# Optimization experiments

Hardware: AMD Instinct MI355X
Metric: run time of the kernel (lower is better)

## Reference

```python
import jax, jax.numpy as jnp
import numpy as np

B, S, D, E, F = 2, 2048, 1024, 8, 4096


def setup_inputs() -> dict:
    key = jax.random.key(0)
    k1, k2, k3, k4 = jax.random.split(key, 4)
    x = jax.random.normal(k1, (B, S, D), dtype=jnp.float32)
    gate_w = jax.random.normal(k2, (E, D), dtype=jnp.float32) * 0.02
    w1 = jax.random.normal(k3, (E, D, F), dtype=jnp.float32) * 0.02
    w2 = jax.random.normal(k4, (E, F, D), dtype=jnp.float32) * 0.02
    return {"x": x, "gate_w": gate_w, "w1": w1, "w2": w2}


def reference(x, gate_w, w1, w2):
    b, s, d = x.shape
    n_experts = w1.shape[0]
    tokens = x.reshape(-1, d)                      # (T, D)
    logits = tokens @ gate_w.T                     # (T, E) router (Linear, no bias)
    expert_ids = jnp.argmax(logits, axis=-1)       # top-1 routing (T,)
    dispatch = jax.nn.one_hot(expert_ids, n_experts, dtype=tokens.dtype)  # (T, E)
    # dense all-experts reference of the grouped GEMM: h_e = tokens @ w1[e]
    h = jnp.einsum('td,edf->etf', tokens, w1)      # (E, T, F)
    h = jax.nn.gelu(h, approximate=False)          # torch F.gelu default = exact erf
    out_e = jnp.einsum('etf,efd->etd', h, w2)      # (E, T, D)
    # scatter back: each token takes exactly its assigned expert's output
    out = jnp.einsum('etd,te->td', out_e, dispatch)
    return out.reshape(b, s, d)
```

## Files before the change

kernel.cpp:

```cpp
#include <hip/hip_runtime.h>
#include <hip/hip_bf16.h>
#include <math.h>

#define T_TOK 4096
#define D_DIM 1024
#define E_EXP 8
#define F_DIM 4096
#define BM 128
#define BN 128
#define BK 32
#define LDK 40
#define MAX_TILES 40
#define KSPLIT 4

typedef __attribute__((ext_vector_type(8))) short short8;
typedef __attribute__((ext_vector_type(4))) short short4v;
typedef __attribute__((ext_vector_type(4))) float float4v;

__device__ __forceinline__ short f2b(float f) {
    union { float f; unsigned u; } v; v.f = f;
    unsigned r = v.u + 0x7fffu + ((v.u >> 16) & 1u);
    return (short)(r >> 16);
}

typedef const __attribute__((address_space(1))) unsigned gu32;
typedef __attribute__((address_space(3))) unsigned lu32;
__device__ __forceinline__ void gload16(const void* g, void* l) {
    __builtin_amdgcn_global_load_lds((gu32*)g, (lu32*)l, 16, 0, 0);
}

__global__ void router_kernel(const float* __restrict__ x, const float* __restrict__ gw,
                              int* __restrict__ eid, int* __restrict__ rnk,
                              int* __restrict__ counts) {
    int lane = threadIdx.x & 63;
    int wave = threadIdx.x >> 6;
    int t = blockIdx.x * 4 + wave;
    const float* xr = x + (size_t)t * D_DIM;
    float p[E_EXP];
#pragma unroll
    for (int e = 0; e < E_EXP; ++e) p[e] = 0.f;
#pragma unroll
    for (int i = 0; i < D_DIM / 64; ++i) {
        float v = xr[lane + 64 * i];
#pragma unroll
        for (int e = 0; e < E_EXP; ++e)
            p[e] = fmaf(v, gw[e * D_DIM + lane + 64 * i], p[e]);
    }
#pragma unroll
    for (int off = 32; off > 0; off >>= 1) {
#pragma unroll
        for (int e = 0; e < E_EXP; ++e) p[e] += __shfl_down(p[e], off, 64);
    }
    if (lane == 0) {
        int best = 0; float bv = p[0];
#pragma unroll
        for (int e = 1; e < E_EXP; ++e) if (p[e] > bv) { bv = p[e]; best = e; }
        eid[t] = best;
        rnk[t] = atomicAdd(&counts[best], 1);
    }
}

__global__ void prefix_kernel(const int* __restrict__ counts, int* __restrict__ offsets,
                              int* __restrict__ tmap) {
    int off = 0;
    offsets[0] = 0;
    int nt = 0;
    for (int e = 0; e < E_EXP; ++e) {
        int c = counts[e];
        for (int m0 = 0; m0 < c; m0 += BM) {
            tmap[nt * 3 + 0] = e;
            tmap[nt * 3 + 1] = off + m0;
            tmap[nt * 3 + 2] = (c - m0 < BM) ? (c - m0) : BM;
            ++nt;
        }
        off += c;
        offsets[e + 1] = off;
    }
    for (; nt < MAX_TILES; ++nt) tmap[nt * 3 + 2] = 0;
}

__global__ void scatter_kernel(const int* __restrict__ eid, const int* __restrict__ rnk,
                               const int* __restrict__ offsets, int* __restrict__ sorted) {
    int t = blockIdx.x * 256 + threadIdx.x;
    sorted[offsets[eid[t]] + rnk[t]] = t;
}

__global__ __launch_bounds__(256) void xcvt_kernel(const float* __restrict__ src,
                                                   short* __restrict__ dst) {
    size_t i = ((size_t)blockIdx.x * 256 + threadIdx.x) * 4;
    float4v v = *(const float4v*)(src + i);
    short4v w;
#pragma unroll
    for (int q = 0; q < 4; ++q) w[q] = f2b(v[q]);
    *(short4v*)(dst + i) = w;
}

__global__ __launch_bounds__(256) void transpose_cvt(const float* __restrict__ src,
                                                     short* __restrict__ dst,
                                                     int R, int C) {
    __shared__ float t[64][65];
    size_t eoff = (size_t)blockIdx.z * R * C;
    const float* s = src + eoff;
    short* d = dst + eoff;
    int c0 = blockIdx.x * 64, r0 = blockIdx.y * 64;
    int tr = threadIdx.x >> 4;
    int tc = (threadIdx.x & 15) * 4;
#pragma unroll
    for (int p = 0; p < 4; ++p) {
        int r = tr + p * 16;
        float4v v = *(const float4v*)(s + (size_t)(r0 + r) * C + (c0 + tc));
        t[r][tc + 0] = v[0]; t[r][tc + 1] = v[1]; t[r][tc + 2] = v[2]; t[r][tc + 3] = v[3];
    }
    __syncthreads();
#pragma unroll
    for (int p = 0; p < 4; ++p) {
        int cl = tr + p * 16;
        short4v w;
#pragma unroll
        for (int q = 0; q < 4; ++q) w[q] = f2b(t[tc + q][cl]);
        *(short4v*)(d + (size_t)(c0 + cl) * R + (r0 + tc)) = w;
    }
}


__global__ __launch_bounds__(256) void gemm1_kernel(const short* __restrict__ xb,
                                                    const short* __restrict__ w1t,
                                                    const int* __restrict__ sorted,
                                                    const int* __restrict__ tmap,
                                                    short* __restrict__ hb) {
    __shared__ __align__(16) short As[4096];
    __shared__ __align__(16) short Bs[4096];
    __shared__ int srow[BM];
    int mt = blockIdx.y;
    int m_count = tmap[mt * 3 + 2];
    if (m_count == 0) return;
    int e = tmap[mt * 3 + 0];
    int row0 = tmap[mt * 3 + 1];
    int n0 = blockIdx.x * BN;
    int tid = threadIdx.x;
    if (tid < BM) srow[tid] = sorted[row0 + (tid < m_count ? tid : m_count - 1)];
    __syncthreads();

    int lane = tid & 63, wave = tid >> 6;
    int wm = (wave & 1) * 64, wn = (wave >> 1) * 64;
    int s0 = 2 * wave, s1 = s0 + 1;
    int c0s = s0 >> 1, m0s = (s0 & 1) * 64 + lane;
    int c1s = s1 >> 1, m1s = (s1 & 1) * 64 + lane;
    const short* aptr0 = xb + (size_t)srow[m0s] * D_DIM + c0s * 8;
    const short* aptr1 = xb + (size_t)srow[m1s] * D_DIM + c1s * 8;
    const short* wbase = w1t + (size_t)e * F_DIM * D_DIM;
    const short* bptr0 = wbase + (size_t)(n0 + m0s) * D_DIM + c0s * 8;
    const short* bptr1 = wbase + (size_t)(n0 + m1s) * D_DIM + c1s * 8;
    short* al0 = &As[s0 * 512];
    short* al1 = &As[s1 * 512];
    short* bl0 = &Bs[s0 * 512];
    short* bl1 = &Bs[s1 * 512];

    float4v acc[4][4];
#pragma unroll
    for (int i = 0; i < 4; ++i)
#pragma unroll
        for (int j = 0; j < 4; ++j) acc[i][j] = (float4v)(0.f);

    int cr = (lane >> 4) * 128;
    int lm = lane & 15;
    for (int k0 = 0; k0 < D_DIM; k0 += BK) {
        gload16(aptr0 + k0, al0);
        gload16(aptr1 + k0, al1);
        gload16(bptr0 + k0, bl0);
        gload16(bptr1 + k0, bl1);
        __syncthreads();
        short8 af[4], bf[4];
#pragma unroll
        for (int i = 0; i < 4; ++i)
            af[i] = *(const short8*)&As[(cr + wm + i * 16 + lm) * 8];
#pragma unroll
        for (int j = 0; j < 4; ++j)
            bf[j] = *(const short8*)&Bs[(cr + wn + j * 16 + lm) * 8];
#pragma unroll
        for (int i = 0; i < 4; ++i)
#pragma unroll
            for (int j = 0; j < 4; ++j)
                acc[i][j] = __builtin_amdgcn_mfma_f32_16x16x32_bf16(af[i], bf[j], acc[i][j], 0, 0, 0);
        __syncthreads();
    }
    int rbase = (lane >> 4) * 4;
    int cbase = lane & 15;
#pragma unroll
    for (int i = 0; i < 4; ++i) {
#pragma unroll
        for (int r = 0; r < 4; ++r) {
            int row = wm + i * 16 + rbase + r;
            if (row < m_count) {
                short* hp = hb + (size_t)(row0 + row) * F_DIM + n0 + wn + cbase;
#pragma unroll
                for (int j = 0; j < 4; ++j) {
                    float s = acc[i][j][r];
                    float g = 0.5f * s * (1.f + erff(s * 0.70710678118f));
                    hp[j * 16] = f2b(g);
                }
            }
        }
    }
}

__global__ __launch_bounds__(256) void gemm2_kernel(const short* __restrict__ hb,
                                                    const short* __restrict__ w2t,
                                                    const int* __restrict__ tmap,
                                                    float* __restrict__ pbuf) {
    __shared__ __align__(16) short As[4096];
    __shared__ __align__(16) short Bs[4096];
    int mt = blockIdx.y;
    int m_count = tmap[mt * 3 + 2];
    if (m_count == 0) return;
    int e = tmap[mt * 3 + 0];
    int row0 = tmap[mt * 3 + 1];
    int n0 = blockIdx.x * BN;
    int kp = blockIdx.z;
    int kbase = kp * (F_DIM / KSPLIT);
    int tid = threadIdx.x;
    int lane = tid & 63, wave = tid >> 6;
    int wm = (wave & 1) * 64, wn = (wave >> 1) * 64;
    int s0 = 2 * wave, s1 = s0 + 1;
    int c0s = s0 >> 1, m0s = (s0 & 1) * 64 + lane;
    int c1s = s1 >> 1, m1s = (s1 & 1) * 64 + lane;
    int am0 = m0s < m_count ? m0s : m_count - 1;
    int am1 = m1s < m_count ? m1s : m_count - 1;
    const short* aptr0 = hb + (size_t)(row0 + am0) * F_DIM + kbase + c0s * 8;
    const short* aptr1 = hb + (size_t)(row0 + am1) * F_DIM + kbase + c1s * 8;
    const short* wbase = w2t + (size_t)e * D_DIM * F_DIM;
    const short* bptr0 = wbase + (size_t)(n0 + m0s) * F_DIM + kbase + c0s * 8;
    const short* bptr1 = wbase + (size_t)(n0 + m1s) * F_DIM + kbase + c1s * 8;
    short* al0 = &As[s0 * 512];
    short* al1 = &As[s1 * 512];
    short* bl0 = &Bs[s0 * 512];
    short* bl1 = &Bs[s1 * 512];

    float4v acc[4][4];
#pragma unroll
    for (int i = 0; i < 4; ++i)
#pragma unroll
        for (int j = 0; j < 4; ++j) acc[i][j] = (float4v)(0.f);

    int cr = (lane >> 4) * 128;
    int lm = lane & 15;
    for (int k0 = 0; k0 < F_DIM / KSPLIT; k0 += BK) {
        gload16(aptr0 + k0, al0);
        gload16(aptr1 + k0, al1);
        gload16(bptr0 + k0, bl0);
        gload16(bptr1 + k0, bl1);
        __syncthreads();
        short8 af[4], bf[4];
#pragma unroll
        for (int i = 0; i < 4; ++i)
            af[i] = *(const short8*)&As[(cr + wm + i * 16 + lm) * 8];
#pragma unroll
        for (int j = 0; j < 4; ++j)
            bf[j] = *(const short8*)&Bs[(cr + wn + j * 16 + lm) * 8];
#pragma unroll
        for (int i = 0; i < 4; ++i)
#pragma unroll
            for (int j = 0; j < 4; ++j)
                acc[i][j] = __builtin_amdgcn_mfma_f32_16x16x32_bf16(af[i], bf[j], acc[i][j], 0, 0, 0);
        __syncthreads();
    }
    float* pb = pbuf + (size_t)kp * T_TOK * D_DIM;
    int rbase = (lane >> 4) * 4;
    int cbase = lane & 15;
#pragma unroll
    for (int i = 0; i < 4; ++i) {
#pragma unroll
        for (int r = 0; r < 4; ++r) {
            int row = wm + i * 16 + rbase + r;
            if (row < m_count) {
                float* pp = pb + (size_t)(row0 + row) * D_DIM + n0 + wn + cbase;
#pragma unroll
                for (int j = 0; j < 4; ++j) pp[j * 16] = acc[i][j][r];
            }
        }
    }
}

__global__ __launch_bounds__(256) void reduce_kernel(const float* __restrict__ pbuf,
                                                     const int* __restrict__ sorted,
                                                     float* __restrict__ out) {
    int s = blockIdx.x;
    int d = threadIdx.x * 4;
    const float* p = pbuf + (size_t)s * D_DIM + d;
    float4v a = *(const float4v*)(p);
    a += *(const float4v*)(p + (size_t)1 * T_TOK * D_DIM);
    a += *(const float4v*)(p + (size_t)2 * T_TOK * D_DIM);
    a += *(const float4v*)(p + (size_t)3 * T_TOK * D_DIM);
    *(float4v*)(out + (size_t)sorted[s] * D_DIM + d) = a;
}

__global__ __launch_bounds__(256) void gemm1_fb(const float* __restrict__ x,
                                                const float* __restrict__ w1,
                                                const int* __restrict__ sorted,
                                                const int* __restrict__ tmap,
                                                short* __restrict__ hbuf) {
    __shared__ short As[BM * LDK];
    __shared__ short Bs[BN * LDK];
    __shared__ int srow[BM];
    int mt = blockIdx.y;
    int m_count = tmap[mt * 3 + 2];
    if (m_count == 0) return;
    int e = tmap[mt * 3 + 0];
    int row0 = tmap[mt * 3 + 1];
    int n0 = blockIdx.x * BN;
    int tid = threadIdx.x;
    if (tid < BM) srow[tid] = sorted[row0 + (tid < m_count ? tid : m_count - 1)];
    __syncthreads();
    int lane = tid & 63, wave = tid >> 6;
    int wm = (wave & 1) * 64, wn = (wave >> 1) * 64;
    float4v acc[4][4];
#pragma unroll
    for (int i = 0; i < 4; ++i)
#pragma unroll
        for (int j = 0; j < 4; ++j) acc[i][j] = (float4v)(0.f);
    int ar = tid >> 1, ac = (tid & 1) * 16, bn = tid & 127, bq = (tid >> 7) * 16;
    const float* abase = x + (size_t)srow[ar] * D_DIM + ac;
    const float* bbase = w1 + (size_t)e * D_DIM * F_DIM + (size_t)bq * F_DIM + (n0 + bn);
    for (int k0 = 0; k0 < D_DIM; k0 += BK) {
        {
            const float* ap = abase + k0;
            float4v f0 = *(const float4v*)(ap);
            float4v f1 = *(const float4v*)(ap + 4);
            float4v f2 = *(const float4v*)(ap + 8);
            float4v f3 = *(const float4v*)(ap + 12);
            short8 t0, t1;
#pragma unroll
            for (int c = 0; c < 4; ++c) {
                t0[c] = f2b(f0[c]); t0[4 + c] = f2b(f1[c]);
                t1[c] = f2b(f2[c]); t1[4 + c] = f2b(f3[c]);
            }
            *(short8*)(&As[ar * LDK + ac]) = t0;
            *(short8*)(&As[ar * LDK + ac + 8]) = t1;
        }
        {
            const float* bp = bbase + (size_t)k0 * F_DIM;
            float v[16];
#pragma unroll
            for (int j = 0; j < 16; ++j) v[j] = bp[(size_t)j * F_DIM];
            short8 t0, t1;
#pragma unroll
            for (int j = 0; j < 8; ++j) { t0[j] = f2b(v[j]); t1[j] = f2b(v[8 + j]); }
            *(short8*)(&Bs[bn * LDK + bq]) = t0;
            *(short8*)(&Bs[bn * LDK + bq + 8]) = t1;
        }
        __syncthreads();
        short8 af[4], bf[4];
#pragma unroll
        for (int i = 0; i < 4; ++i)
            af[i] = *(const short8*)(&As[(wm + i * 16 + (lane & 15)) * LDK + (lane >> 4) * 8]);
#pragma unroll
        for (int j = 0; j < 4; ++j)
            bf[j] = *(const short8*)(&Bs[(wn + j * 16 + (lane & 15)) * LDK + (lane >> 4) * 8]);
#pragma unroll
        for (int i = 0; i < 4; ++i)
#pragma unroll
            for (int j = 0; j < 4; ++j)
                acc[i][j] = __builtin_amdgcn_mfma_f32_16x16x32_bf16(af[i], bf[j], acc[i][j], 0, 0, 0);
        __syncthreads();
    }
    int rbase = (lane >> 4) * 4, cbase = lane & 15;
#pragma unroll
    for (int i = 0; i < 4; ++i) {
#pragma unroll
        for (int r = 0; r < 4; ++r) {
            int row = wm + i * 16 + rbase + r;
            if (row < m_count) {
                short* hp = hbuf + (size_t)(row0 + row) * F_DIM + n0 + wn + cbase;
#pragma unroll
                for (int j = 0; j < 4; ++j) {
                    float s = acc[i][j][r];
                    float g = 0.5f * s * (1.f + erff(s * 0.70710678118f));
                    hp[j * 16] = f2b(g);
                }
            }
        }
    }
}

__global__ __launch_bounds__(256) void gemm2_fb(const short* __restrict__ hbuf,
                                                const float* __restrict__ w2,
                                                const int* __restrict__ sorted,
                                                const int* __restrict__ tmap,
                                                float* __restrict__ out) {
    __shared__ short As[BM * LDK];
    __shared__ short Bs[BN * LDK];
    __shared__ int srow[BM];
    int mt = blockIdx.y;
    int m_count = tmap[mt * 3 + 2];
    if (m_count == 0) return;
    int e = tmap[mt * 3 + 0];
    int row0 = tmap[mt * 3 + 1];
    int n0 = blockIdx.x * BN;
    int tid = threadIdx.x;
    if (tid < BM) srow[tid] = sorted[row0 + (tid < m_count ? tid : m_count - 1)];
    __syncthreads();
    int lane = tid & 63, wave = tid >> 6;
    int wm = (wave & 1) * 64, wn = (wave >> 1) * 64;
    float4v acc[4][4];
#pragma unroll
    for (int i = 0; i < 4; ++i)
#pragma unroll
        for (int j = 0; j < 4; ++j) acc[i][j] = (float4v)(0.f);
    int ar = tid >> 1, ac = (tid & 1) * 16, bn = tid & 127, bq = (tid >> 7) * 16;
    int arc = ar < m_count ? ar : m_count - 1;
    const short* abase = hbuf + (size_t)(row0 + arc) * F_DIM + ac;
    const float* bbase = w2 + (size_t)e * F_DIM * D_DIM + (size_t)bq * D_DIM + (n0 + bn);
    for (int k0 = 0; k0 < F_DIM; k0 += BK) {
        {
            const short* ap = abase + k0;
            *(short8*)(&As[ar * LDK + ac]) = *(const short8*)(ap);
            *(short8*)(&As[ar * LDK + ac + 8]) = *(const short8*)(ap + 8);
        }
        {
            const float* bp = bbase + (size_t)k0 * D_DIM;
            float v[16];
#pragma unroll
            for (int j = 0; j < 16; ++j) v[j] = bp[(size_t)j * D_DIM];
            short8 t0, t1;
#pragma unroll
            for (int j = 0; j < 8; ++j) { t0[j] = f2b(v[j]); t1[j] = f2b(v[8 + j]); }
            *(short8*)(&Bs[bn * LDK + bq]) = t0;
            *(short8*)(&Bs[bn * LDK + bq + 8]) = t1;
        }
        __syncthreads();
        short8 af[4], bf[4];
#pragma unroll
        for (int i = 0; i < 4; ++i)
            af[i] = *(const short8*)(&As[(wm + i * 16 + (lane & 15)) * LDK + (lane >> 4) * 8]);
#pragma unroll
        for (int j = 0; j < 4; ++j)
            bf[j] = *(const short8*)(&Bs[(wn + j * 16 + (lane & 15)) * LDK + (lane >> 4) * 8]);
#pragma unroll
        for (int i = 0; i < 4; ++i)
#pragma unroll
            for (int j = 0; j < 4; ++j)
                acc[i][j] = __builtin_amdgcn_mfma_f32_16x16x32_bf16(af[i], bf[j], acc[i][j], 0, 0, 0);
        __syncthreads();
    }
    int rbase = (lane >> 4) * 4, cbase = lane & 15;
#pragma unroll
    for (int i = 0; i < 4; ++i) {
#pragma unroll
        for (int r = 0; r < 4; ++r) {
            int row = wm + i * 16 + rbase + r;
            if (row < m_count) {
                float* op = out + (size_t)srow[row] * D_DIM + n0 + wn + cbase;
#pragma unroll
                for (int j = 0; j < 4; ++j) op[j * 16] = acc[i][j][r];
            }
        }
    }
}

extern "C" void kernel_launch(void* const* d_in, const int* in_sizes, int n_in,
                              void* d_out, int out_size, void* d_ws, size_t ws_size,
                              hipStream_t stream) {
    const float* x  = (const float*)d_in[0];
    const float* gw = (const float*)d_in[1];
    const float* w1 = (const float*)d_in[2];
    const float* w2 = (const float*)d_in[3];
    float* out = (float*)d_out;
    char* ws = (char*)d_ws;

    int* counts  = (int*)(ws);
    int* offsets = (int*)(ws + 64);
    int* tmap    = (int*)(ws + 128);
    int* eid     = (int*)(ws + 1024);
    int* rnk     = (int*)(ws + 17408);
    int* sorted  = (int*)(ws + 33792);

    const size_t XB_OFF  = 65536;
    const size_t W1T_OFF = XB_OFF  + (size_t)T_TOK * D_DIM * 2;
    const size_t W2T_OFF = W1T_OFF + (size_t)E_EXP * D_DIM * F_DIM * 2;
    const size_t HB_OFF  = W2T_OFF + (size_t)E_EXP * D_DIM * F_DIM * 2;
    const size_t PB_OFF  = HB_OFF  + (size_t)T_TOK * F_DIM * 2;
    const size_t NEED    = PB_OFF  + (size_t)KSPLIT * T_TOK * D_DIM * 4;

    hipMemsetAsync(counts, 0, 32, stream);
    router_kernel<<<T_TOK / 4, 256, 0, stream>>>(x, gw, eid, rnk, counts);
    prefix_kernel<<<1, 1, 0, stream>>>(counts, offsets, tmap);
    scatter_kernel<<<T_TOK / 256, 256, 0, stream>>>(eid, rnk, offsets, sorted);

    if (ws_size >= NEED) {
        short* xb   = (short*)(ws + XB_OFF);
        short* w1t  = (short*)(ws + W1T_OFF);
        short* w2t  = (short*)(ws + W2T_OFF);
        short* hb   = (short*)(ws + HB_OFF);
        float* pbuf = (float*)(ws + PB_OFF);
        xcvt_kernel<<<(T_TOK * D_DIM) / 1024, 256, 0, stream>>>(x, xb);
        transpose_cvt<<<dim3(F_DIM / 64, D_DIM / 64, E_EXP), 256, 0, stream>>>(w1, w1t, D_DIM, F_DIM);
        transpose_cvt<<<dim3(D_DIM / 64, F_DIM / 64, E_EXP), 256, 0, stream>>>(w2, w2t, F_DIM, D_DIM);
        gemm1_kernel<<<dim3(F_DIM / BN, MAX_TILES), 256, 0, stream>>>(xb, w1t, sorted, tmap, hb);
        gemm2_kernel<<<dim3(D_DIM / BN, MAX_TILES, KSPLIT), 256, 0, stream>>>(hb, w2t, tmap, pbuf);
        reduce_kernel<<<T_TOK, 256, 0, stream>>>(pbuf, sorted, out);
    } else {
        short* hbuf = (short*)(ws + 51200);
        gemm1_fb<<<dim3(F_DIM / BN, MAX_TILES), 256, 0, stream>>>(x, w1, sorted, tmap, hbuf);
        gemm2_fb<<<dim3(D_DIM / BN, MAX_TILES), 256, 0, stream>>>(hbuf, w2, sorted, tmap, out);
    }
}
```

Before: 600.9 us.

## Fuse x conversion into router, drop prefix kernel, double K step in GEMMs

Several changes land together. The bf16 conversion of x moves into the router kernel, and the separate prefix kernel is replaced by an inline tile lookup over the per-expert counts, which removes two launches. Both bf16 GEMMs now stage a K=64 slice per barrier pair, using two LDS halves and halving the number of sync iterations at the cost of doubled LDS. The transpose kernel is reworked to write 16-element contiguous bf16 runs per thread instead of 4-element ones.

Result: faster. 587.4 us (-2.2%).

```diff
diff --git a/kernel.cpp b/kernel.cpp
--- a/kernel.cpp
+++ b/kernel.cpp
@@ -8,8 +8,7 @@
 #define F_DIM 4096
 #define BM 128
 #define BN 128
-#define BK 32
-#define LDK 40
+#define BK2 64
 #define MAX_TILES 40
 #define KSPLIT 4
 
@@ -29,19 +28,40 @@
     __builtin_amdgcn_global_load_lds((gu32*)g, (lu32*)l, 16, 0, 0);
 }
 
+__device__ __forceinline__ bool tile_lookup(const int* __restrict__ counts, int mt,
+                                            int& e, int& row0, int& m_count) {
+    int off = 0, acc = 0;
+#pragma unroll
+    for (int i = 0; i < E_EXP; ++i) {
+        int c = counts[i];
+        int nt = (c + BM - 1) >> 7;
+        if (mt < acc + nt) {
+            int j = mt - acc;
+            e = i; row0 = off + j * BM;
+            int mc = c - j * BM;
+            m_count = mc > BM ? BM : mc;
+            return true;
+        }
+        acc += nt; off += c;
+    }
+    return false;
+}
+
 __global__ void router_kernel(const float* __restrict__ x, const float* __restrict__ gw,
                               int* __restrict__ eid, int* __restrict__ rnk,
-                              int* __restrict__ counts) {
+                              int* __restrict__ counts, short* __restrict__ xb) {
     int lane = threadIdx.x & 63;
     int wave = threadIdx.x >> 6;
     int t = blockIdx.x * 4 + wave;
     const float* xr = x + (size_t)t * D_DIM;
+    short* xbr = xb + (size_t)t * D_DIM;
     float p[E_EXP];
 #pragma unroll
     for (int e = 0; e < E_EXP; ++e) p[e] = 0.f;
 #pragma unroll
     for (int i = 0; i < D_DIM / 64; ++i) {
         float v = xr[lane + 64 * i];
+        xbr[lane + 64 * i] = f2b(v);
 #pragma unroll
         for (int e = 0; e < E_EXP; ++e)
             p[e] = fmaf(v, gw[e * D_DIM + lane + 64 * i], p[e]);
@@ -60,39 +80,14 @@
     }
 }
 
-__global__ void prefix_kernel(const int* __restrict__ counts, int* __restrict__ offsets,
-                              int* __restrict__ tmap) {
+__global__ void scatter_kernel(const int* __restrict__ eid, const int* __restrict__ rnk,
+                               const int* __restrict__ counts, int* __restrict__ sorted) {
+    int t = blockIdx.x * 256 + threadIdx.x;
+    int e = eid[t];
     int off = 0;
-    offsets[0] = 0;
-    int nt = 0;
-    for (int e = 0; e < E_EXP; ++e) {
-        int c = counts[e];
-        for (int m0 = 0; m0 < c; m0 += BM) {
-            tmap[nt * 3 + 0] = e;
-            tmap[nt * 3 + 1] = off + m0;
-            tmap[nt * 3 + 2] = (c - m0 < BM) ? (c - m0) : BM;
-            ++nt;
-        }
-        off += c;
-        offsets[e + 1] = off;
-    }
-    for (; nt < MAX_TILES; ++nt) tmap[nt * 3 + 2] = 0;
-}
-
-__global__ void scatter_kernel(const int* __restrict__ eid, const int* __restrict__ rnk,
-                               const int* __restrict__ offsets, int* __restrict__ sorted) {
-    int t = blockIdx.x * 256 + threadIdx.x;
-    sorted[offsets[eid[t]] + rnk[t]] = t;
-}
-
-__global__ __launch_bounds__(256) void xcvt_kernel(const float* __restrict__ src,
-                                                   short* __restrict__ dst) {
-    size_t i = ((size_t)blockIdx.x * 256 + threadIdx.x) * 4;
-    float4v v = *(const float4v*)(src + i);
-    short4v w;
-#pragma unroll
-    for (int q = 0; q < 4; ++q) w[q] = f2b(v[q]);
-    *(short4v*)(dst + i) = w;
+#pragma unroll
+    for (int i = 0; i < E_EXP; ++i) off += (i < e) ? counts[i] : 0;
+    sorted[off + rnk[t]] = t;
 }
 
 __global__ __launch_bounds__(256) void transpose_cvt(const float* __restrict__ src,
@@ -109,33 +104,30 @@
     for (int p = 0; p < 4; ++p) {
         int r = tr + p * 16;
         float4v v = *(const float4v*)(s + (size_t)(r0 + r) * C + (c0 + tc));
-        t[r][tc + 0] = v[0]; t[r][tc + 1] = v[1]; t[r][tc + 2] = v[2]; t[r][tc + 3] = v[3];
+        t[tc + 0][r] = v[0]; t[tc + 1][r] = v[1]; t[tc + 2][r] = v[2]; t[tc + 3][r] = v[3];
     }
     __syncthreads();
-#pragma unroll
-    for (int p = 0; p < 4; ++p) {
-        int cl = tr + p * 16;
-        short4v w;
-#pragma unroll
-        for (int q = 0; q < 4; ++q) w[q] = f2b(t[tc + q][cl]);
-        *(short4v*)(d + (size_t)(c0 + cl) * R + (r0 + tc)) = w;
-    }
+    int nl = threadIdx.x >> 2;
+    int kl = (threadIdx.x & 3) * 16;
+    short8 w0, w1;
+#pragma unroll
+    for (int q = 0; q < 8; ++q) { w0[q] = f2b(t[nl][kl + q]); w1[q] = f2b(t[nl][kl + 8 + q]); }
+    short* dp = d + (size_t)(c0 + nl) * R + (r0 + kl);
+    *(short8*)(dp) = w0;
+    *(short8*)(dp + 8) = w1;
 }
 
 
 __global__ __launch_bounds__(256) void gemm1_kernel(const short* __restrict__ xb,
                                                     const short* __restrict__ w1t,
                                                     const int* __restrict__ sorted,
-                                                    const int* __restrict__ tmap,
+                                                    const int* __restrict__ counts,
                                                     short* __restrict__ hb) {
-    __shared__ __align__(16) short As[4096];
-    __shared__ __align__(16) short Bs[4096];
+    __shared__ __align__(16) short As[8192];
+    __shared__ __align__(16) short Bs[8192];
     __shared__ int srow[BM];
-    int mt = blockIdx.y;
-    int m_count = tmap[mt * 3 + 2];
-    if (m_count == 0) return;
-    int e = tmap[mt * 3 + 0];
-    int row0 = tmap[mt * 3 + 1];
+    int e, row0, m_count;
+    if (!tile_lookup(counts, blockIdx.y, e, row0, m_count)) return;
     int n0 = blockIdx.x * BN;
     int tid = threadIdx.x;
     if (tid < BM) srow[tid] = sorted[row0 + (tid < m_count ? tid : m_count - 1)];
@@ -143,18 +135,19 @@
 
     int lane = tid & 63, wave = tid >> 6;
     int wm = (wave & 1) * 64, wn = (wave >> 1) * 64;
-    int s0 = 2 * wave, s1 = s0 + 1;
-    int c0s = s0 >> 1, m0s = (s0 & 1) * 64 + lane;
-    int c1s = s1 >> 1, m1s = (s1 & 1) * 64 + lane;
-    const short* aptr0 = xb + (size_t)srow[m0s] * D_DIM + c0s * 8;
-    const short* aptr1 = xb + (size_t)srow[m1s] * D_DIM + c1s * 8;
-    const short* wbase = w1t + (size_t)e * F_DIM * D_DIM;
-    const short* bptr0 = wbase + (size_t)(n0 + m0s) * D_DIM + c0s * 8;
-    const short* bptr1 = wbase + (size_t)(n0 + m1s) * D_DIM + c1s * 8;
-    short* al0 = &As[s0 * 512];
-    short* al1 = &As[s1 * 512];
-    short* bl0 = &Bs[s0 * 512];
-    short* bl1 = &Bs[s1 * 512];
+    const short* aA0 = xb + (size_t)srow[lane] * D_DIM + wave * 8;
+    const short* aA1 = xb + (size_t)srow[64 + lane] * D_DIM + wave * 8;
+    const short* wb = w1t + (size_t)e * F_DIM * D_DIM;
+    const short* aB0 = wb + (size_t)(n0 + lane) * D_DIM + wave * 8;
+    const short* aB1 = wb + (size_t)(n0 + 64 + lane) * D_DIM + wave * 8;
+    short* lA00 = &As[(wave * 128) * 8];
+    short* lA01 = &As[(wave * 128 + 64) * 8];
+    short* lA10 = &As[4096 + (wave * 128) * 8];
+    short* lA11 = &As[4096 + (wave * 128 + 64) * 8];
+    short* lB00 = &Bs[(wave * 128) * 8];
+    short* lB01 = &Bs[(wave * 128 + 64) * 8];
+    short* lB10 = &Bs[4096 + (wave * 128) * 8];
+    short* lB11 = &Bs[4096 + (wave * 128 + 64) * 8];
 
     float4v acc[4][4];
 #pragma unroll
@@ -164,24 +157,27 @@
 
     int cr = (lane >> 4) * 128;
     int lm = lane & 15;
-    for (int k0 = 0; k0 < D_DIM; k0 += BK) {
-        gload16(aptr0 + k0, al0);
-        gload16(aptr1 + k0, al1);
-        gload16(bptr0 + k0, bl0);
-        gload16(bptr1 + k0, bl1);
-        __syncthreads();
-        short8 af[4], bf[4];
-#pragma unroll
-        for (int i = 0; i < 4; ++i)
-            af[i] = *(const short8*)&As[(cr + wm + i * 16 + lm) * 8];
-#pragma unroll
-        for (int j = 0; j < 4; ++j)
-            bf[j] = *(const short8*)&Bs[(cr + wn + j * 16 + lm) * 8];
-#pragma unroll
-        for (int i = 0; i < 4; ++i)
+    for (int k0 = 0; k0 < D_DIM; k0 += BK2) {
+        gload16(aA0 + k0, lA00);      gload16(aA1 + k0, lA01);
+        gload16(aA0 + k0 + 32, lA10); gload16(aA1 + k0 + 32, lA11);
+        gload16(aB0 + k0, lB00);      gload16(aB1 + k0, lB01);
+        gload16(aB0 + k0 + 32, lB10); gload16(aB1 + k0 + 32, lB11);
+        __syncthreads();
+#pragma unroll
+        for (int h = 0; h < 2; ++h) {
+            short8 af[4], bf[4];
+#pragma unroll
+            for (int i = 0; i < 4; ++i)
+                af[i] = *(const short8*)&As[h * 4096 + (cr + wm + i * 16 + lm) * 8];
 #pragma unroll
             for (int j = 0; j < 4; ++j)
-                acc[i][j] = __builtin_amdgcn_mfma_f32_16x16x32_bf16(af[i], bf[j], acc[i][j], 0, 0, 0);
+                bf[j] = *(const short8*)&Bs[h * 4096 + (cr + wn + j * 16 + lm) * 8];
+#pragma unroll
+            for (int i = 0; i < 4; ++i)
+#pragma unroll
+                for (int j = 0; j < 4; ++j)
+                    acc[i][j] = __builtin_amdgcn_mfma_f32_16x16x32_bf16(af[i], bf[j], acc[i][j], 0, 0, 0);
+        }
         __syncthreads();
     }
     int rbase = (lane >> 4) * 4;
@@ -206,35 +202,33 @@
 
 __global__ __launch_bounds__(256) void gemm2_kernel(const short* __restrict__ hb,
                                                     const short* __restrict__ w2t,
-                                                    const int* __restrict__ tmap,
+                                                    const int* __restrict__ counts,
                                                     float* __restrict__ pbuf) {
-    __shared__ __align__(16) short As[4096];
-    __shared__ __align__(16) short Bs[4096];
-    int mt = blockIdx.y;
-    int m_count = tmap[mt * 3 + 2];
-    if (m_count == 0) return;
-    int e = tmap[mt * 3 + 0];
-    int row0 = tmap[mt * 3 + 1];
+    __shared__ __align__(16) short As[8192];
+    __shared__ __align__(16) short Bs[8192];
+    int e, row0, m_count;
+    if (!tile_lookup(counts, blockIdx.y, e, row0, m_count)) return;
     int n0 = blockIdx.x * BN;
     int kp = blockIdx.z;
     int kbase = kp * (F_DIM / KSPLIT);
     int tid = threadIdx.x;
     int lane = tid & 63, wave = tid >> 6;
     int wm = (wave & 1) * 64, wn = (wave >> 1) * 64;
-    int s0 = 2 * wave, s1 = s0 + 1;
-    int c0s = s0 >> 1, m0s = (s0 & 1) * 64 + lane;
-    int c1s = s1 >> 1, m1s = (s1 & 1) * 64 + lane;
-    int am0 = m0s < m_count ? m0s : m_count - 1;
-    int am1 = m1s < m_count ? m1s : m_count - 1;
-    const short* aptr0 = hb + (size_t)(row0 + am0) * F_DIM + kbase + c0s * 8;
-    const short* aptr1 = hb + (size_t)(row0 + am1) * F_DIM + kbase + c1s * 8;
-    const short* wbase = w2t + (size_t)e * D_DIM * F_DIM;
-    const short* bptr0 = wbase + (size_t)(n0 + m0s) * F_DIM + kbase + c0s * 8;
-    const short* bptr1 = wbase + (size_t)(n0 + m1s) * F_DIM + kbase + c1s * 8;
-    short* al0 = &As[s0 * 512];
-    short* al1 = &As[s1 * 512];
-    short* bl0 = &Bs[s0 * 512];
-    short* bl1 = &Bs[s1 * 512];
+    int am0 = lane < m_count ? lane : m_count - 1;
+    int am1 = (64 + lane) < m_count ? (64 + lane) : m_count - 1;
+    const short* aA0 = hb + (size_t)(row0 + am0) * F_DIM + kbase + wave * 8;
+    const short* aA1 = hb + (size_t)(row0 + am1) * F_DIM + kbase + wave * 8;
+    const short* wb = w2t + (size_t)e * D_DIM * F_DIM;
+    const short* aB0 = wb + (size_t)(n0 + lane) * F_DIM + kbase + wave * 8;
+    const short* aB1 = wb + (size_t)(n0 + 64 + lane) * F_DIM + kbase + wave * 8;
+    short* lA00 = &As[(wave * 128) * 8];
+    short* lA01 = &As[(wave * 128 + 64) * 8];
+    short* lA10 = &As[4096 + (wave * 128) * 8];
+    short* lA11 = &As[4096 + (wave * 128 + 64) * 8];
+    short* lB00 = &Bs[(wave * 128) * 8];
+    short* lB01 = &Bs[(wave * 128 + 64) * 8];
+    short* lB10 = &Bs[4096 + (wave * 128) * 8];
+    short* lB11 = &Bs[4096 + (wave * 128 + 64) * 8];
 
     float4v acc[4][4];
 #pragma unroll
@@ -244,24 +238,28 @@
 
     int cr = (lane >> 4) * 128;
     int lm = lane & 15;
-    for (int k0 = 0; k0 < F_DIM / KSPLIT; k0 += BK) {
-        gload16(aptr0 + k0, al0);
-        gload16(aptr1 + k0, al1);
-        gload16(bptr0 + k0, bl0);
-        gload16(bptr1 + k0, bl1);
-        __syncthreads();
-        short8 af[4], bf[4];
-#pragma unroll
-        for (int i = 0; i < 4; ++i)
-            af[i] = *(const short8*)&As[(cr + wm + i * 16 + lm) * 8];
-#pragma unroll
-        for (int j = 0; j < 4; ++j)
-            bf[j] = *(const short8*)&Bs[(cr + wn + j * 16 + lm) * 8];
-#pragma unroll
-        for (int i = 0; i < 4; ++i)
+    const int KLEN = F_DIM / KSPLIT;
+    for (int k0 = 0; k0 < KLEN; k0 += BK2) {
+        gload16(aA0 + k0, lA00);      gload16(aA1 + k0, lA01);
+        gload16(aA0 + k0 + 32, lA10); gload16(aA1 + k0 + 32, lA11);
+        gload16(aB0 + k0, lB00);      gload16(aB1 + k0, lB01);
+        gload16(aB0 + k0 + 32, lB10); gload16(aB1 + k0 + 32, lB11);
+        __syncthreads();
+#pragma unroll
+        for (int h = 0; h < 2; ++h) {
+            short8 af[4], bf[4];
+#pragma unroll
+            for (int i = 0; i < 4; ++i)
+                af[i] = *(const short8*)&As[h * 4096 + (cr + wm + i * 16 + lm) * 8];
 #pragma unroll
             for (int j = 0; j < 4; ++j)
-                acc[i][j] = __builtin_amdgcn_mfma_f32_16x16x32_bf16(af[i], bf[j], acc[i][j], 0, 0, 0);
+                bf[j] = *(const short8*)&Bs[h * 4096 + (cr + wn + j * 16 + lm) * 8];
+#pragma unroll
+            for (int i = 0; i < 4; ++i)
+#pragma unroll
+                for (int j = 0; j < 4; ++j)
+                    acc[i][j] = __builtin_amdgcn_mfma_f32_16x16x32_bf16(af[i], bf[j], acc[i][j], 0, 0, 0);
+        }
         __syncthreads();
     }
     float* pb = pbuf + (size_t)kp * T_TOK * D_DIM;
@@ -294,19 +292,17 @@
     *(float4v*)(out + (size_t)sorted[s] * D_DIM + d) = a;
 }
 
+#define LDK 40
 __global__ __launch_bounds__(256) void gemm1_fb(const float* __restrict__ x,
                                                 const float* __restrict__ w1,
                                                 const int* __restrict__ sorted,
-                                                const int* __restrict__ tmap,
+                                                const int* __restrict__ counts,
                                                 short* __restrict__ hbuf) {
     __shared__ short As[BM * LDK];
     __shared__ short Bs[BN * LDK];
     __shared__ int srow[BM];
-    int mt = blockIdx.y;
-    int m_count = tmap[mt * 3 + 2];
-    if (m_count == 0) return;
-    int e = tmap[mt * 3 + 0];
-    int row0 = tmap[mt * 3 + 1];
+    int e, row0, m_count;
+    if (!tile_lookup(counts, blockIdx.y, e, row0, m_count)) return;
     int n0 = blockIdx.x * BN;
     int tid = threadIdx.x;
     if (tid < BM) srow[tid] = sorted[row0 + (tid < m_count ? tid : m_count - 1)];
@@ -321,7 +317,7 @@
     int ar = tid >> 1, ac = (tid & 1) * 16, bn = tid & 127, bq = (tid >> 7) * 16;
     const float* abase = x + (size_t)srow[ar] * D_DIM + ac;
     const float* bbase = w1 + (size_t)e * D_DIM * F_DIM + (size_t)bq * F_DIM + (n0 + bn);
-    for (int k0 = 0; k0 < D_DIM; k0 += BK) {
+    for (int k0 = 0; k0 < D_DIM; k0 += 32) {
         {
             const float* ap = abase + k0;
             float4v f0 = *(const float4v*)(ap);
@@ -385,16 +381,13 @@
 __global__ __launch_bounds__(256) void gemm2_fb(const short* __restrict__ hbuf,
                                                 const float* __restrict__ w2,
                                                 const int* __restrict__ sorted,
-                                                const int* __restrict__ tmap,
+                                                const int* __restrict__ counts,
                                                 float* __restrict__ out) {
     __shared__ short As[BM * LDK];
     __shared__ short Bs[BN * LDK];
     __shared__ int srow[BM];
-    int mt = blockIdx.y;
-    int m_count = tmap[mt * 3 + 2];
-    if (m_count == 0) return;
-    int e = tmap[mt * 3 + 0];
-    int row0 = tmap[mt * 3 + 1];
+    int e, row0, m_count;
+    if (!tile_lookup(counts, blockIdx.y, e, row0, m_count)) return;
     int n0 = blockIdx.x * BN;
     int tid = threadIdx.x;
     if (tid < BM) srow[tid] = sorted[row0 + (tid < m_count ? tid : m_count - 1)];
@@ -410,7 +403,7 @@
     int arc = ar < m_count ? ar : m_count - 1;
     const short* abase = hbuf + (size_t)(row0 + arc) * F_DIM + ac;
     const float* bbase = w2 + (size_t)e * F_DIM * D_DIM + (size_t)bq * D_DIM + (n0 + bn);
-    for (int k0 = 0; k0 < F_DIM; k0 += BK) {
+    for (int k0 = 0; k0 < F_DIM; k0 += 32) {
         {
             const short* ap = abase + k0;
             *(short8*)(&As[ar * LDK + ac]) = *(const short8*)(ap);
@@ -467,12 +460,10 @@
     float* out = (float*)d_out;
     char* ws = (char*)d_ws;
 
-    int* counts  = (int*)(ws);
-    int* offsets = (int*)(ws + 64);
-    int* tmap    = (int*)(ws + 128);
-    int* eid     = (int*)(ws + 1024);
-    int* rnk     = (int*)(ws + 17408);
-    int* sorted  = (int*)(ws + 33792);
+    int* counts = (int*)(ws);
+    int* eid    = (int*)(ws + 1024);
+    int* rnk    = (int*)(ws + 17408);
+    int* sorted = (int*)(ws + 33792);
 
     const size_t XB_OFF  = 65536;
     const size_t W1T_OFF = XB_OFF  + (size_t)T_TOK * D_DIM * 2;
@@ -481,26 +472,25 @@
     const size_t PB_OFF  = HB_OFF  + (size_t)T_TOK * F_DIM * 2;
     const size_t NEED    = PB_OFF  + (size_t)KSPLIT * T_TOK * D_DIM * 4;
 
+    short* xb = (short*)(ws + XB_OFF);
+
     hipMemsetAsync(counts, 0, 32, stream);
-    router_kernel<<<T_TOK / 4, 256, 0, stream>>>(x, gw, eid, rnk, counts);
-    prefix_kernel<<<1, 1, 0, stream>>>(counts, offsets, tmap);
-    scatter_kernel<<<T_TOK / 256, 256, 0, stream>>>(eid, rnk, offsets, sorted);
+    router_kernel<<<T_TOK / 4, 256, 0, stream>>>(x, gw, eid, rnk, counts, xb);
+    scatter_kernel<<<T_TOK / 256, 256, 0, stream>>>(eid, rnk, counts, sorted);
 
     if (ws_size >= NEED) {
-        short* xb   = (short*)(ws + XB_OFF);
         short* w1t  = (short*)(ws + W1T_OFF);
         short* w2t  = (short*)(ws + W2T_OFF);
         short* hb   = (short*)(ws + HB_OFF);
         float* pbuf = (float*)(ws + PB_OFF);
-        xcvt_kernel<<<(T_TOK * D_DIM) / 1024, 256, 0, stream>>>(x, xb);
         transpose_cvt<<<dim3(F_DIM / 64, D_DIM / 64, E_EXP), 256, 0, stream>>>(w1, w1t, D_DIM, F_DIM);
         transpose_cvt<<<dim3(D_DIM / 64, F_DIM / 64, E_EXP), 256, 0, stream>>>(w2, w2t, F_DIM, D_DIM);
-        gemm1_kernel<<<dim3(F_DIM / BN, MAX_TILES), 256, 0, stream>>>(xb, w1t, sorted, tmap, hb);
-        gemm2_kernel<<<dim3(D_DIM / BN, MAX_TILES, KSPLIT), 256, 0, stream>>>(hb, w2t, tmap, pbuf);
+        gemm1_kernel<<<dim3(F_DIM / BN, MAX_TILES), 256, 0, stream>>>(xb, w1t, sorted, counts, hb);
+        gemm2_kernel<<<dim3(D_DIM / BN, MAX_TILES, KSPLIT), 256, 0, stream>>>(hb, w2t, counts, pbuf);
         reduce_kernel<<<T_TOK, 256, 0, stream>>>(pbuf, sorted, out);
     } else {
         short* hbuf = (short*)(ws + 51200);
-        gemm1_fb<<<dim3(F_DIM / BN, MAX_TILES), 256, 0, stream>>>(x, w1, sorted, tmap, hbuf);
-        gemm2_fb<<<dim3(D_DIM / BN, MAX_TILES), 256, 0, stream>>>(hbuf, w2, sorted, tmap, out);
-    }
-}
+        gemm1_fb<<<dim3(F_DIM / BN, MAX_TILES), 256, 0, stream>>>(x, w1, sorted, counts, hbuf);
+        gemm2_fb<<<dim3(D_DIM / BN, MAX_TILES), 256, 0, stream>>>(hbuf, w2, sorted, counts, out);
+    }
+}
```
